# Kernel optimization log

Measured on AMD Instinct MI355X. Metric: run time of the kernel, lower is better.

The kernel has to match this reference:

```python
import jax, jax.numpy as jnp
import numpy as np

S, B = 16384, 1
E = 2048          # encoder_hidden_size * num_enc_direction
H = 1024          # decoder_hidden_size
L = 2             # num_layer_dec
C = 5             # num_classes


def setup_inputs() -> dict:
    key = jax.random.key(0)
    ks = jax.random.split(key, 16)
    s = lambda fan_in: 1.0 / np.sqrt(fan_in)
    inp = {
        "encoder_hiddens": jax.random.normal(ks[0], (S, B, E), jnp.float32),
        "hidden": jax.random.normal(ks[1], (L, B, H), jnp.float32),
        "c": jax.random.normal(ks[2], (L, B, H), jnp.float32),
        # attn_alpha: Linear(2H + E, 1)
        "attn_w": jax.random.uniform(ks[3], (1, 2 * H + E), jnp.float32, -s(2 * H + E), s(2 * H + E)),
        "attn_b": jax.random.uniform(ks[4], (1,), jnp.float32, -s(2 * H + E), s(2 * H + E)),
        # LSTM layer 0: input E -> H
        "w_ih_l0": jax.random.uniform(ks[5], (4 * H, E), jnp.float32, -s(H), s(H)),
        "w_hh_l0": jax.random.uniform(ks[6], (4 * H, H), jnp.float32, -s(H), s(H)),
        "b_ih_l0": jax.random.uniform(ks[7], (4 * H,), jnp.float32, -s(H), s(H)),
        "b_hh_l0": jax.random.uniform(ks[8], (4 * H,), jnp.float32, -s(H), s(H)),
        # LSTM layer 1: input H -> H
        "w_ih_l1": jax.random.uniform(ks[9], (4 * H, H), jnp.float32, -s(H), s(H)),
        "w_hh_l1": jax.random.uniform(ks[10], (4 * H, H), jnp.float32, -s(H), s(H)),
        "b_ih_l1": jax.random.uniform(ks[11], (4 * H,), jnp.float32, -s(H), s(H)),
        "b_hh_l1": jax.random.uniform(ks[12], (4 * H,), jnp.float32, -s(H), s(H)),
        # fc: Linear(H, C)
        "fc_w": jax.random.uniform(ks[13], (C, H), jnp.float32, -s(H), s(H)),
        "fc_b": jax.random.uniform(ks[14], (C,), jnp.float32, -s(H), s(H)),
    }
    return inp


def _lstm_cell(x, h, c, w_ih, w_hh, b_ih, b_hh):
    # PyTorch gate order: i, f, g, o
    gates = x @ w_ih.T + b_ih + h @ w_hh.T + b_hh  # [B, 4H]
    i, f, g, o = jnp.split(gates, 4, axis=-1)
    c2 = jax.nn.sigmoid(f) * c + jax.nn.sigmoid(i) * jnp.tanh(g)
    h2 = jax.nn.sigmoid(o) * jnp.tanh(c2)
    return h2, c2


def reference(encoder_hiddens, hidden, c, attn_w, attn_b,
              w_ih_l0, w_hh_l0, b_ih_l0, b_hh_l0,
              w_ih_l1, w_hh_l1, b_ih_l1, b_hh_l1,
              fc_w, fc_b):
    h0, c0 = hidden[0], c[0]  # [B, H]
    # Vectorized per-timestep attn_alpha(concat(h0, c0, enc_i)):
    # split attn_w columns over [h0 | c0 | enc] and fuse the static part.
    w_h, w_c, w_e = attn_w[:, :H], attn_w[:, H:2 * H], attn_w[:, 2 * H:]
    static = h0 @ w_h.T + c0 @ w_c.T + attn_b            # [B, 1]
    scores = jnp.einsum('sbe,oe->sbo', encoder_hiddens, w_e) + static  # [S, B, 1]
    # Original applies softmax over dim=1 of a [B=1, 1] tensor per step -> all ones.
    attn = jax.nn.softmax(scores, axis=-1)               # [S, B, 1], identically 1.0
    # bmm(enc[B,E,S], attn[B,S,1]) == weighted sum over S
    attn_applied = jnp.einsum('sbe,sb->be', encoder_hiddens, attn[..., 0])  # [B, E]

    # 2-layer LSTM, single timestep
    h1, c1 = _lstm_cell(attn_applied, hidden[0], c[0], w_ih_l0, w_hh_l0, b_ih_l0, b_hh_l0)
    h2, c2 = _lstm_cell(h1, hidden[1], c[1], w_ih_l1, w_hh_l1, b_ih_l1, b_hh_l1)

    out = h2  # [B, H] == out.view(1*B, H)
    return out @ fc_w.T + fc_b  # [B, C]
```

## Files before the change

kernel.cpp:

```cpp
#include <hip/hip_runtime.h>
#include <hip/hip_bf16.h>
#include <math.h>

#define S_LEN 16384
#define E_DIM 2048
#define H_DIM 1024
#define G_DIM 4096
#define C_DIM 5

#define RCH 128
#define ROWS_PER_CHUNK (S_LEN / RCH)

#define WS_PART   0
#define WS_COLSUM (WS_PART + RCH * E_DIM)
#define WS_G0     (WS_COLSUM + E_DIM)
#define WS_H1     (WS_G0 + G_DIM)
#define WS_G1     (WS_H1 + H_DIM)
#define WS_H2     (WS_G1 + G_DIM)

__global__ __launch_bounds__(256) void colsum_partial_k(
    const float4* __restrict__ enc, float4* __restrict__ part) {
  const int E4 = E_DIM / 4;
  int colgroup = blockIdx.x & 1;
  int chunk = blockIdx.x >> 1;
  int e4 = colgroup * 256 + threadIdx.x;
  float4 acc = {0.f, 0.f, 0.f, 0.f};
  int r0 = chunk * ROWS_PER_CHUNK;
#pragma unroll 4
  for (int r = r0; r < r0 + ROWS_PER_CHUNK; ++r) {
    float4 v = enc[(size_t)r * E4 + e4];
    acc.x += v.x; acc.y += v.y; acc.z += v.z; acc.w += v.w;
  }
  part[chunk * E4 + e4] = acc;
}

__global__ __launch_bounds__(256) void colsum_final_k(
    const float4* __restrict__ part, float4* __restrict__ colsum) {
  const int E4 = E_DIM / 4;
  int e4 = blockIdx.x * blockDim.x + threadIdx.x;
  if (e4 >= E4) return;
  float4 acc = {0.f, 0.f, 0.f, 0.f};
  for (int ch = 0; ch < RCH; ++ch) {
    float4 v = part[ch * E4 + e4];
    acc.x += v.x; acc.y += v.y; acc.z += v.z; acc.w += v.w;
  }
  colsum[e4] = acc;
}

__global__ __launch_bounds__(256) void gates_k(
    const float4* __restrict__ w_ih, const float4* __restrict__ w_hh,
    const float* __restrict__ b_ih, const float* __restrict__ b_hh,
    const float4* __restrict__ x, int xlen4,
    const float4* __restrict__ h, int hlen4,
    float* __restrict__ gates) {
  int wave = threadIdx.x >> 6;
  int lane = threadIdx.x & 63;
  int row = blockIdx.x * 4 + wave;

  float acc = 0.f;
  const float4* wi = w_ih + (size_t)row * xlen4;
  for (int k = lane; k < xlen4; k += 64) {
    float4 w4 = wi[k];
    float4 v = x[k];
    acc += w4.x * v.x + w4.y * v.y + w4.z * v.z + w4.w * v.w;
  }
  const float4* wh = w_hh + (size_t)row * hlen4;
  for (int k = lane; k < hlen4; k += 64) {
    float4 w4 = wh[k];
    float4 v = h[k];
    acc += w4.x * v.x + w4.y * v.y + w4.z * v.z + w4.w * v.w;
  }
#pragma unroll
  for (int off = 32; off > 0; off >>= 1) acc += __shfl_down(acc, off);
  if (lane == 0) gates[row] = acc + b_ih[row] + b_hh[row];
}

__global__ __launch_bounds__(256) void cell_k(
    const float* __restrict__ gates, const float* __restrict__ c_prev,
    float* __restrict__ h_out) {
  int j = blockIdx.x * blockDim.x + threadIdx.x;
  if (j >= H_DIM) return;
  float ig = gates[j];
  float fg = gates[H_DIM + j];
  float gg = gates[2 * H_DIM + j];
  float og = gates[3 * H_DIM + j];
  float si = 1.f / (1.f + expf(-ig));
  float sf = 1.f / (1.f + expf(-fg));
  float so = 1.f / (1.f + expf(-og));
  float c2 = sf * c_prev[j] + si * tanhf(gg);
  h_out[j] = so * tanhf(c2);
}

__global__ __launch_bounds__(320) void fc_k(
    const float4* __restrict__ fc_w, const float* __restrict__ fc_b,
    const float4* __restrict__ h2, float* __restrict__ out) {
  int wave = threadIdx.x >> 6;
  int lane = threadIdx.x & 63;
  if (wave >= C_DIM) return;
  const int H4 = H_DIM / 4;
  float acc = 0.f;
  const float4* wr = fc_w + (size_t)wave * H4;
  for (int k = lane; k < H4; k += 64) {
    float4 w4 = wr[k];
    float4 v = h2[k];
    acc += w4.x * v.x + w4.y * v.y + w4.z * v.z + w4.w * v.w;
  }
#pragma unroll
  for (int off = 32; off > 0; off >>= 1) acc += __shfl_down(acc, off);
  if (lane == 0) out[wave] = acc + fc_b[wave];
}

extern "C" void kernel_launch(void* const* d_in, const int* in_sizes, int n_in,
                              void* d_out, int out_size, void* d_ws, size_t ws_size,
                              hipStream_t stream) {
  const float* enc     = (const float*)d_in[0];
  const float* hidden  = (const float*)d_in[1];
  const float* c_in    = (const float*)d_in[2];
  const float* w_ih_l0 = (const float*)d_in[5];
  const float* w_hh_l0 = (const float*)d_in[6];
  const float* b_ih_l0 = (const float*)d_in[7];
  const float* b_hh_l0 = (const float*)d_in[8];
  const float* w_ih_l1 = (const float*)d_in[9];
  const float* w_hh_l1 = (const float*)d_in[10];
  const float* b_ih_l1 = (const float*)d_in[11];
  const float* b_hh_l1 = (const float*)d_in[12];
  const float* fc_w    = (const float*)d_in[13];
  const float* fc_b    = (const float*)d_in[14];

  float* ws = (float*)d_ws;
  float* part   = ws + WS_PART;
  float* colsum = ws + WS_COLSUM;
  float* g0     = ws + WS_G0;
  float* h1     = ws + WS_H1;
  float* g1     = ws + WS_G1;
  float* h2     = ws + WS_H2;
  float* out    = (float*)d_out;

  colsum_partial_k<<<2 * RCH, 256, 0, stream>>>((const float4*)enc, (float4*)part);
  colsum_final_k<<<2, 256, 0, stream>>>((const float4*)part, (float4*)colsum);

  gates_k<<<G_DIM / 4, 256, 0, stream>>>(
      (const float4*)w_ih_l0, (const float4*)w_hh_l0, b_ih_l0, b_hh_l0,
      (const float4*)colsum, E_DIM / 4, (const float4*)hidden, H_DIM / 4, g0);
  cell_k<<<H_DIM / 256, 256, 0, stream>>>(g0, c_in, h1);

  gates_k<<<G_DIM / 4, 256, 0, stream>>>(
      (const float4*)w_ih_l1, (const float4*)w_hh_l1, b_ih_l1, b_hh_l1,
      (const float4*)h1, H_DIM / 4, (const float4*)(hidden + H_DIM), H_DIM / 4, g1);
  cell_k<<<H_DIM / 256, 256, 0, stream>>>(g1, c_in + H_DIM, h2);

  fc_k<<<1, 320, 0, stream>>>((const float4*)fc_w, fc_b, (const float4*)h2, out);
}
```

Baseline: 54.34 us.

## Fuse LSTM gate GEMV with cell update and widen colsum reduction

Result: slower. 62.03 us (+14.2%).

```diff
diff --git a/kernel.cpp b/kernel.cpp
--- a/kernel.cpp
+++ b/kernel.cpp
@@ -8,15 +8,13 @@
 #define G_DIM 4096
 #define C_DIM 5
 
-#define RCH 128
+#define RCH 256
 #define ROWS_PER_CHUNK (S_LEN / RCH)
 
 #define WS_PART   0
 #define WS_COLSUM (WS_PART + RCH * E_DIM)
-#define WS_G0     (WS_COLSUM + E_DIM)
-#define WS_H1     (WS_G0 + G_DIM)
-#define WS_G1     (WS_H1 + H_DIM)
-#define WS_H2     (WS_G1 + G_DIM)
+#define WS_H1     (WS_COLSUM + E_DIM)
+#define WS_H2     (WS_H1 + H_DIM)
 
 __global__ __launch_bounds__(256) void colsum_partial_k(
     const float4* __restrict__ enc, float4* __restrict__ part) {
@@ -26,7 +24,7 @@
   int e4 = colgroup * 256 + threadIdx.x;
   float4 acc = {0.f, 0.f, 0.f, 0.f};
   int r0 = chunk * ROWS_PER_CHUNK;
-#pragma unroll 4
+#pragma unroll 8
   for (int r = r0; r < r0 + ROWS_PER_CHUNK; ++r) {
     float4 v = enc[(size_t)r * E4 + e4];
     acc.x += v.x; acc.y += v.y; acc.z += v.z; acc.w += v.w;
@@ -35,36 +33,37 @@
 }
 
 __global__ __launch_bounds__(256) void colsum_final_k(
-    const float4* __restrict__ part, float4* __restrict__ colsum) {
-  const int E4 = E_DIM / 4;
-  int e4 = blockIdx.x * blockDim.x + threadIdx.x;
-  if (e4 >= E4) return;
-  float4 acc = {0.f, 0.f, 0.f, 0.f};
-  for (int ch = 0; ch < RCH; ++ch) {
-    float4 v = part[ch * E4 + e4];
-    acc.x += v.x; acc.y += v.y; acc.z += v.z; acc.w += v.w;
-  }
-  colsum[e4] = acc;
+    const float* __restrict__ part, float* __restrict__ colsum) {
+  int e = blockIdx.x * blockDim.x + threadIdx.x;
+  float acc = 0.f;
+#pragma unroll 8
+  for (int ch = 0; ch < RCH; ++ch) acc += part[(size_t)ch * E_DIM + e];
+  colsum[e] = acc;
 }
 
-__global__ __launch_bounds__(256) void gates_k(
+__global__ __launch_bounds__(256) void lstm_fused_k(
     const float4* __restrict__ w_ih, const float4* __restrict__ w_hh,
     const float* __restrict__ b_ih, const float* __restrict__ b_hh,
     const float4* __restrict__ x, int xlen4,
     const float4* __restrict__ h, int hlen4,
-    float* __restrict__ gates) {
+    const float* __restrict__ c_prev,
+    float* __restrict__ h_out) {
+  __shared__ float smem[4];
   int wave = threadIdx.x >> 6;
   int lane = threadIdx.x & 63;
-  int row = blockIdx.x * 4 + wave;
+  int j = blockIdx.x;
+  int row = wave * H_DIM + j;
 
   float acc = 0.f;
   const float4* wi = w_ih + (size_t)row * xlen4;
+#pragma unroll
   for (int k = lane; k < xlen4; k += 64) {
     float4 w4 = wi[k];
     float4 v = x[k];
     acc += w4.x * v.x + w4.y * v.y + w4.z * v.z + w4.w * v.w;
   }
   const float4* wh = w_hh + (size_t)row * hlen4;
+#pragma unroll
   for (int k = lane; k < hlen4; k += 64) {
     float4 w4 = wh[k];
     float4 v = h[k];
@@ -72,23 +71,16 @@
   }
 #pragma unroll
   for (int off = 32; off > 0; off >>= 1) acc += __shfl_down(acc, off);
-  if (lane == 0) gates[row] = acc + b_ih[row] + b_hh[row];
-}
-
-__global__ __launch_bounds__(256) void cell_k(
-    const float* __restrict__ gates, const float* __restrict__ c_prev,
-    float* __restrict__ h_out) {
-  int j = blockIdx.x * blockDim.x + threadIdx.x;
-  if (j >= H_DIM) return;
-  float ig = gates[j];
-  float fg = gates[H_DIM + j];
-  float gg = gates[2 * H_DIM + j];
-  float og = gates[3 * H_DIM + j];
-  float si = 1.f / (1.f + expf(-ig));
-  float sf = 1.f / (1.f + expf(-fg));
-  float so = 1.f / (1.f + expf(-og));
-  float c2 = sf * c_prev[j] + si * tanhf(gg);
-  h_out[j] = so * tanhf(c2);
+  if (lane == 0) smem[wave] = acc + b_ih[row] + b_hh[row];
+  __syncthreads();
+  if (threadIdx.x == 0) {
+    float ig = smem[0], fg = smem[1], gg = smem[2], og = smem[3];
+    float si = 1.f / (1.f + expf(-ig));
+    float sf = 1.f / (1.f + expf(-fg));
+    float so = 1.f / (1.f + expf(-og));
+    float c2 = sf * c_prev[j] + si * tanhf(gg);
+    h_out[j] = so * tanhf(c2);
+  }
 }
 
 __global__ __launch_bounds__(320) void fc_k(
@@ -100,6 +92,7 @@
   const int H4 = H_DIM / 4;
   float acc = 0.f;
   const float4* wr = fc_w + (size_t)wave * H4;
+#pragma unroll
   for (int k = lane; k < H4; k += 64) {
     float4 w4 = wr[k];
     float4 v = h2[k];
@@ -130,24 +123,22 @@
   float* ws = (float*)d_ws;
   float* part   = ws + WS_PART;
   float* colsum = ws + WS_COLSUM;
-  float* g0     = ws + WS_G0;
   float* h1     = ws + WS_H1;
-  float* g1     = ws + WS_G1;
   float* h2     = ws + WS_H2;
   float* out    = (float*)d_out;
 
   colsum_partial_k<<<2 * RCH, 256, 0, stream>>>((const float4*)enc, (float4*)part);
-  colsum_final_k<<<2, 256, 0, stream>>>((const float4*)part, (float4*)colsum);
+  colsum_final_k<<<E_DIM / 256, 256, 0, stream>>>(part, colsum);
 
-  gates_k<<<G_DIM / 4, 256, 0, stream>>>(
+  lstm_fused_k<<<H_DIM, 256, 0, stream>>>(
       (const float4*)w_ih_l0, (const float4*)w_hh_l0, b_ih_l0, b_hh_l0,
-      (const float4*)colsum, E_DIM / 4, (const float4*)hidden, H_DIM / 4, g0);
-  cell_k<<<H_DIM / 256, 256, 0, stream>>>(g0, c_in, h1);
+      (const float4*)colsum, E_DIM / 4, (const float4*)hidden, H_DIM / 4,
+      c_in, h1);
 
-  gates_k<<<G_DIM / 4, 256, 0, stream>>>(
+  lstm_fused_k<<<H_DIM, 256, 0, stream>>>(
       (const float4*)w_ih_l1, (const float4*)w_hh_l1, b_ih_l1, b_hh_l1,
-      (const float4*)h1, H_DIM / 4, (const float4*)(hidden + H_DIM), H_DIM / 4, g1);
-  cell_k<<<H_DIM / 256, 256, 0, stream>>>(g1, c_in + H_DIM, h2);
+      (const float4*)h1, H_DIM / 4, (const float4*)(hidden + H_DIM), H_DIM / 4,
+      c_in + H_DIM, h2);
 
   fc_k<<<1, 320, 0, stream>>>((const float4*)fc_w, fc_b, (const float4*)h2, out);
 }
```
